# Optimization experiments

Hardware: AMD Instinct MI355X
Metric: run time of the kernel (lower is better)

## Reference

```python
import jax, jax.numpy as jnp
import numpy as np

D_MODEL = 1024
N_HEADS = 16
HEAD_DIM = D_MODEL // N_HEADS  # 64
WINDOW = 64
HALF = WINDOW // 2  # query i attends keys in [i-HALF, i+HALF]
CHUNK = WINDOW      # chunk size for banded attention; must be >= HALF and divide S
B, S = 4, 4096


def setup_inputs() -> dict:
    key = jax.random.key(0)
    ks = jax.random.split(key, 6)
    s = 0.02
    D = D_MODEL
    return {
        "x":  jax.random.normal(ks[0], (B, S, D), jnp.float32),
        "Wq": jax.random.normal(ks[1], (D, D), jnp.float32) * s,
        "bq": jnp.zeros((D,), jnp.float32),
        "Wk": jax.random.normal(ks[2], (D, D), jnp.float32) * s,
        "bk": jnp.zeros((D,), jnp.float32),
        "Wv": jax.random.normal(ks[3], (D, D), jnp.float32) * s,
        "bv": jnp.zeros((D,), jnp.float32),
        "Wo": jax.random.normal(ks[4], (D, D), jnp.float32) * s,
        "bo": jnp.zeros((D,), jnp.float32),
    }


def reference(x, Wq, bq, Wk, bk, Wv, bv, Wo, bo):
    # Sliding-window attention (seq_len > 128 path of SparseAttention).
    b, s, d = x.shape
    h, hd = N_HEADS, HEAD_DIM
    scale = 1.0 / np.sqrt(hd).astype(np.float32)

    q = (x @ Wq.T + bq).reshape(b, s, h, hd)
    k = (x @ Wk.T + bk).reshape(b, s, h, hd)
    v = (x @ Wv.T + bv).reshape(b, s, h, hd)

    c = CHUNK
    nb = s // c
    qc = q.reshape(b, nb, c, h, hd)

    # Pad one chunk of zeros on each side; each query chunk attends keys in
    # chunks [n-1, n, n+1] (covers the +/-HALF band since HALF <= c).
    pad = jnp.zeros((b, c, h, hd), q.dtype)
    kp = jnp.concatenate([pad, k, pad], axis=1).reshape(b, nb + 2, c, h, hd)
    vp = jnp.concatenate([pad, v, pad], axis=1).reshape(b, nb + 2, c, h, hd)
    k3 = jnp.concatenate([kp[:, :-2], kp[:, 1:-1], kp[:, 2:]], axis=2)  # [b,nb,3c,h,hd]
    v3 = jnp.concatenate([vp[:, :-2], vp[:, 1:-1], vp[:, 2:]], axis=2)

    # scores: [b,h,nb,c,3c]
    scores = jnp.einsum('bnqhd,bnkhd->bhnqk', qc, k3) * scale

    # Banded validity mask. Global query pos = n*c + i ; global key pos = n*c + j - c.
    i = jnp.arange(c)[:, None]          # [c,1]
    j = jnp.arange(3 * c)[None, :]      # [1,3c]
    rel = j - c - i                     # key_pos - query_pos, [c,3c]
    band = (rel >= -HALF) & (rel <= HALF)
    n = jnp.arange(nb)[:, None, None]   # [nb,1,1]
    keypos = n * c + (j - c)[None, :, :]  # [nb,1,3c]
    valid = band[None, :, :] & (keypos >= 0) & (keypos < s)  # [nb,c,3c]

    attn = jax.nn.softmax(jnp.where(valid[None, None], scores, -jnp.inf), axis=-1)
    ctx = jnp.einsum('bhnqk,bnkhd->bnqhd', attn, v3).reshape(b, s, d)
    return ctx @ Wo.T + bo
```

## Files before the change

kernel.cpp:

```cpp
#include <hip/hip_runtime.h>
#include <hip/hip_bf16.h>
#include <cstdint>
#include <cstddef>

#define D_MODEL 1024
#define NHEADS  16
#define HDIM    64
#define HALFW   32
#define BATCH   4
#define SEQ     4096
#define MROWS   (BATCH*SEQ)

typedef __attribute__((ext_vector_type(8))) short        bf16x8;
typedef __attribute__((ext_vector_type(4))) float        f32x4;
typedef __attribute__((ext_vector_type(4))) unsigned int u32x4;

typedef const __attribute__((address_space(1))) void gvoid_t;
typedef __attribute__((address_space(3))) void       lvoid_t;

__device__ __forceinline__ unsigned short f2bf(float f) {
    unsigned int u = __float_as_uint(f);
    u += 0x7fffu + ((u >> 16) & 1u);
    return (unsigned short)(u >> 16);
}

__device__ __forceinline__ int vswz(int row, int bytecol) {
    return (row * 256 + bytecol) ^ (((row ^ (row >> 3)) & 7) << 4);
}

__global__ __launch_bounds__(256)
void cvt_f32_bf16(const float* __restrict__ src, unsigned short* __restrict__ dst, int n8) {
    int i = blockIdx.x * 256 + threadIdx.x;
    if (i >= n8) return;
    float4 a = *(const float4*)(src + (size_t)i * 8);
    float4 b = *(const float4*)(src + (size_t)i * 8 + 4);
    u32x4 o;
    o[0] = (unsigned)f2bf(a.x) | ((unsigned)f2bf(a.y) << 16);
    o[1] = (unsigned)f2bf(a.z) | ((unsigned)f2bf(a.w) << 16);
    o[2] = (unsigned)f2bf(b.x) | ((unsigned)f2bf(b.y) << 16);
    o[3] = (unsigned)f2bf(b.z) | ((unsigned)f2bf(b.w) << 16);
    *(u32x4*)(dst + (size_t)i * 8) = o;
}

__global__ __launch_bounds__(256)
void cvt4_f32_bf16(const float* __restrict__ s0, const float* __restrict__ s1,
                   const float* __restrict__ s2, const float* __restrict__ s3,
                   unsigned short* __restrict__ d0, unsigned short* __restrict__ d1,
                   unsigned short* __restrict__ d2, unsigned short* __restrict__ d3, int n8) {
    int i = blockIdx.x * 256 + threadIdx.x;
    if (i >= n8) return;
    const float* src = blockIdx.y == 0 ? s0 : blockIdx.y == 1 ? s1 : blockIdx.y == 2 ? s2 : s3;
    unsigned short* dst = blockIdx.y == 0 ? d0 : blockIdx.y == 1 ? d1 : blockIdx.y == 2 ? d2 : d3;
    float4 a = *(const float4*)(src + (size_t)i * 8);
    float4 b = *(const float4*)(src + (size_t)i * 8 + 4);
    u32x4 o;
    o[0] = (unsigned)f2bf(a.x) | ((unsigned)f2bf(a.y) << 16);
    o[1] = (unsigned)f2bf(a.z) | ((unsigned)f2bf(a.w) << 16);
    o[2] = (unsigned)f2bf(b.x) | ((unsigned)f2bf(b.y) << 16);
    o[3] = (unsigned)f2bf(b.z) | ((unsigned)f2bf(b.w) << 16);
    *(u32x4*)(dst + (size_t)i * 8) = o;
}

template <int NOUT, int F32OUT>
__global__ __launch_bounds__(512)
void gemm256(const unsigned short* __restrict__ A,
             const unsigned short* __restrict__ W0,
             const unsigned short* __restrict__ W1,
             const unsigned short* __restrict__ W2,
             const float* __restrict__ b0, const float* __restrict__ b1,
             const float* __restrict__ b2,
             unsigned short* __restrict__ o0, unsigned short* __restrict__ o1,
             unsigned short* __restrict__ o2, float* __restrict__ of32)
{
    constexpr int K  = 1024;
    constexpr int NT = K / 64;
    constexpr int NWG = 64 * 4 * NOUT;
    __shared__ unsigned short lds[65536];

    const int tid  = threadIdx.x;
    const int wave = tid >> 6, lane = tid & 63;
    const int wr = wave >> 2, wc = wave & 3;

    const int bid = blockIdx.x;
    const int g   = (bid & 7) * (NWG / 8) + (bid >> 3);
    const int rb  = g / (4 * NOUT);
    const int cb  = g % (4 * NOUT);
    const int which = cb >> 2;
    const int bm = rb * 256, bn = (cb & 3) * 256;

    const unsigned short* W = (NOUT == 1 || which == 0) ? W0 : (which == 1 ? W1 : W2);
    const float* bias       = (NOUT == 1 || which == 0) ? b0 : (which == 1 ? b1 : b2);
    unsigned short* obf     = (NOUT == 1 || which == 0) ? o0 : (which == 1 ? o1 : o2);

    f32x4 acc[8][4];
    #pragma unroll
    for (int m = 0; m < 8; ++m)
        #pragma unroll
        for (int n = 0; n < 4; ++n)
            #pragma unroll
            for (int j = 0; j < 4; ++j) acc[m][n][j] = 0.0f;

    char* ldsb = (char*)lds;

    const int idx0 = tid, idx1 = tid + 512;
    const int r0 = idx0 >> 2, r1 = idx1 >> 2;
    const int c0 = ((idx0 & 3) - (r0 >> 1)) & 3;
    const int c1 = ((idx1 & 3) - (r1 >> 1)) & 3;
    const size_t sA0 = (size_t)(bm + r0) * K + c0 * 8;
    const size_t sA1 = (size_t)(bm + r1) * K + c1 * 8;
    const size_t sB0 = (size_t)(bn + r0) * K + c0 * 8;
    const size_t sB1 = (size_t)(bn + r1) * K + c1 * 8;
    const int ldsW = wave * 1024;

    auto STAGE = [&](int t, int kh, int isA) {
        const int slot = ((t << 1) + kh) & 3;
        const int base = (isA ? 0 : 65536) + slot * 16384 + ldsW;
        const int ke = t * 64 + kh * 32;
        const unsigned short* M = isA ? A : W;
        const size_t s0 = isA ? sA0 : sB0;
        const size_t s1 = isA ? sA1 : sB1;
        __builtin_amdgcn_global_load_lds((gvoid_t*)(M + s0 + ke),
            (lvoid_t*)(ldsb + base), 16, 0, 0);
        __builtin_amdgcn_global_load_lds((gvoid_t*)(M + s1 + ke),
            (lvoid_t*)(ldsb + base + 8192), 16, 0, 0);
    };

    const int lr = lane & 15;
    const int pp = (((lane >> 4) + (lr >> 1)) & 3) << 4;
    const int abase = (wr * 128 + lr) * 64 + pp;
    const int bbase = 65536 + (wc * 64 + lr) * 64 + pp;

    STAGE(0, 0, 1); STAGE(0, 0, 0); STAGE(0, 1, 1); STAGE(0, 1, 0);
    asm volatile("s_waitcnt vmcnt(4)" ::: "memory");
    __builtin_amdgcn_s_barrier();

    #pragma unroll 1
    for (int t = 0; t < NT; ++t) {
        const int more = (t + 1 < NT);
        {
            const int so = (((t << 1) + 0) & 3) * 16384;
            if (more) STAGE(t + 1, 0, 1);
            bf16x8 a[8], b2_[2];
            #pragma unroll
            for (int m = 0; m < 8; ++m) a[m] = *(const bf16x8*)(ldsb + so + abase + m * 1024);
            #pragma unroll
            for (int n = 0; n < 2; ++n) b2_[n] = *(const bf16x8*)(ldsb + so + bbase + n * 1024);
            __builtin_amdgcn_s_barrier();
            __builtin_amdgcn_s_setprio(1);
            #pragma unroll
            for (int m = 0; m < 8; ++m)
                #pragma unroll
                for (int n = 0; n < 2; ++n)
                    acc[m][n] = __builtin_amdgcn_mfma_f32_16x16x32_bf16(a[m], b2_[n], acc[m][n], 0, 0, 0);
            __builtin_amdgcn_s_setprio(0);
            __builtin_amdgcn_s_barrier();
            if (more) STAGE(t + 1, 0, 0);
            #pragma unroll
            for (int n = 0; n < 2; ++n) b2_[n] = *(const bf16x8*)(ldsb + so + bbase + (n + 2) * 1024);
            __builtin_amdgcn_s_barrier();
            __builtin_amdgcn_s_setprio(1);
            #pragma unroll
            for (int m = 0; m < 8; ++m)
                #pragma unroll
                for (int n = 0; n < 2; ++n)
                    acc[m][n + 2] = __builtin_amdgcn_mfma_f32_16x16x32_bf16(a[m], b2_[n], acc[m][n + 2], 0, 0, 0);
            __builtin_amdgcn_s_setprio(0);
            if (more) { asm volatile("s_waitcnt vmcnt(4)" ::: "memory"); }
            else      { asm volatile("s_waitcnt vmcnt(0)" ::: "memory"); }
            __builtin_amdgcn_s_barrier();
        }
        {
            const int so = (((t << 1) + 1) & 3) * 16384;
            if (more) STAGE(t + 1, 1, 1);
            bf16x8 a[8], b2_[2];
            #pragma unroll
            for (int m = 0; m < 8; ++m) a[m] = *(const bf16x8*)(ldsb + so + abase + m * 1024);
            #pragma unroll
            for (int n = 0; n < 2; ++n) b2_[n] = *(const bf16x8*)(ldsb + so + bbase + n * 1024);
            __builtin_amdgcn_s_barrier();
            __builtin_amdgcn_s_setprio(1);
            #pragma unroll
            for (int m = 0; m < 8; ++m)
                #pragma unroll
                for (int n = 0; n < 2; ++n)
                    acc[m][n] = __builtin_amdgcn_mfma_f32_16x16x32_bf16(a[m], b2_[n], acc[m][n], 0, 0, 0);
            __builtin_amdgcn_s_setprio(0);
            __builtin_amdgcn_s_barrier();
            if (more) STAGE(t + 1, 1, 0);
            #pragma unroll
            for (int n = 0; n < 2; ++n) b2_[n] = *(const bf16x8*)(ldsb + so + bbase + (n + 2) * 1024);
            __builtin_amdgcn_s_barrier();
            __builtin_amdgcn_s_setprio(1);
            #pragma unroll
            for (int m = 0; m < 8; ++m)
                #pragma unroll
                for (int n = 0; n < 2; ++n)
                    acc[m][n + 2] = __builtin_amdgcn_mfma_f32_16x16x32_bf16(a[m], b2_[n], acc[m][n + 2], 0, 0, 0);
            __builtin_amdgcn_s_setprio(0);
            if (t + 2 < NT) { asm volatile("s_waitcnt vmcnt(4)" ::: "memory"); }
            else            { asm volatile("s_waitcnt vmcnt(0)" ::: "memory"); }
            __builtin_amdgcn_s_barrier();
        }
    }

    float bvv[4];
    #pragma unroll
    for (int n = 0; n < 4; ++n) bvv[n] = bias[bn + wc * 64 + n * 16 + lr];
    #pragma unroll
    for (int m = 0; m < 8; ++m) {
        #pragma unroll
        for (int j = 0; j < 4; ++j) {
            const int row = bm + wr * 128 + m * 16 + (lane >> 4) * 4 + j;
            #pragma unroll
            for (int n = 0; n < 4; ++n) {
                const int col = bn + wc * 64 + n * 16 + lr;
                const float v = acc[m][n][j] + bvv[n];
                if (F32OUT) of32[(size_t)row * 1024 + col] = v;
                else        obf[(size_t)row * 1024 + col]  = f2bf(v);
            }
        }
    }
}

__global__ __launch_bounds__(256)
void attn_band(const unsigned short* __restrict__ Q,
               const unsigned short* __restrict__ Kk,
               const unsigned short* __restrict__ V,
               unsigned short* __restrict__ Ctx)
{
    __shared__ unsigned short Qs[64 * 72];
    __shared__ unsigned short Ks[128 * 72];
    __shared__ unsigned short Vt[64 * 128];
    __shared__ unsigned short Ps[64 * 128];

    const int qt = blockIdx.x, h = blockIdx.y, b = blockIdx.z;
    const int qbase  = qt * 64;
    const int kstart = qbase - HALFW;
    const int tid = threadIdx.x, wave = tid >> 6, lane = tid & 63;

    const size_t base = (size_t)b * SEQ * D_MODEL + (size_t)h * HDIM;
    const unsigned short* Qb = Q  + base;
    const unsigned short* Kb = Kk + base;
    const unsigned short* Vb = V  + base;
    unsigned short*       Cb = Ctx + base;

    for (int c = tid; c < 512; c += 256) {
        const int row = c >> 3, col = (c & 7) * 8;
        *(u32x4*)(Qs + row * 72 + col) =
            *(const u32x4*)(Qb + (size_t)(qbase + row) * D_MODEL + col);
    }
    for (int c = tid; c < 1024; c += 256) {
        const int krow = c >> 3, col = (c & 7) * 8;
        const int kpos = kstart + krow;
        u32x4 kv;
        if (kpos >= 0 && kpos < SEQ) {
            kv = *(const u32x4*)(Kb + (size_t)kpos * D_MODEL + col);
        } else {
            for (int j = 0; j < 4; ++j) kv[j] = 0u;
        }
        *(u32x4*)(Ks + krow * 72 + col) = kv;
    }
    for (int c = tid; c < 512; c += 256) {
        const int p = c >> 3, dch = c & 7;
        const int k0 = kstart + 2 * p, k1 = k0 + 1;
        u32x4 v0, v1;
        if (k0 >= 0 && k0 < SEQ) {
            v0 = *(const u32x4*)(Vb + (size_t)k0 * D_MODEL + dch * 8);
        } else {
            for (int j = 0; j < 4; ++j) v0[j] = 0u;
        }
        if (k1 >= 0 && k1 < SEQ) {
            v1 = *(const u32x4*)(Vb + (size_t)k1 * D_MODEL + dch * 8);
        } else {
            for (int j = 0; j < 4; ++j) v1[j] = 0u;
        }
        #pragma unroll
        for (int j = 0; j < 8; ++j) {
            const int d = dch * 8 + j;
            const unsigned lo = (v0[j >> 1] >> ((j & 1) * 16)) & 0xffffu;
            const unsigned hi = (v1[j >> 1] >> ((j & 1) * 16)) & 0xffffu;
            *(unsigned*)((char*)Vt + vswz(d, 4 * p)) = lo | (hi << 16);
        }
    }
    __syncthreads();

    f32x4 sc[8];
    #pragma unroll
    for (int c = 0; c < 8; ++c)
        #pragma unroll
        for (int j = 0; j < 4; ++j) sc[c][j] = 0.0f;

    bf16x8 aq[2];
    #pragma unroll
    for (int kc = 0; kc < 2; ++kc)
        aq[kc] = *(const bf16x8*)(Qs + (wave * 16 + (lane & 15)) * 72 + kc * 32 + (lane >> 4) * 8);
    #pragma unroll
    for (int c = 0; c < 8; ++c) {
        #pragma unroll
        for (int kc = 0; kc < 2; ++kc) {
            bf16x8 bk_ = *(const bf16x8*)(Ks + (c * 16 + (lane & 15)) * 72 + kc * 32 + (lane >> 4) * 8);
            sc[c] = __builtin_amdgcn_mfma_f32_16x16x32_bf16(aq[kc], bk_, sc[c], 0, 0, 0);
        }
    }

    const int grp = lane >> 4, colk = lane & 15;
    float rowmax[4] = {-1e30f, -1e30f, -1e30f, -1e30f};
    #pragma unroll
    for (int c = 0; c < 8; ++c) {
        const int kpos = kstart + c * 16 + colk;
        #pragma unroll
        for (int j = 0; j < 4; ++j) {
            const int qpos = qbase + wave * 16 + grp * 4 + j;
            const int rel = kpos - qpos;
            const bool valid = (kpos >= 0) && (kpos < SEQ) && (rel >= -HALFW) && (rel <= HALFW);
            const float v = valid ? sc[c][j] * 0.125f : -1e30f;
            sc[c][j] = v;
            rowmax[j] = fmaxf(rowmax[j], v);
        }
    }
    #pragma unroll
    for (int j = 0; j < 4; ++j)
        #pragma unroll
        for (int m = 1; m < 16; m <<= 1)
            rowmax[j] = fmaxf(rowmax[j], __shfl_xor(rowmax[j], m, 64));

    float rowsum[4] = {0.f, 0.f, 0.f, 0.f};
    #pragma unroll
    for (int c = 0; c < 8; ++c)
        #pragma unroll
        for (int j = 0; j < 4; ++j) {
            const float p = __expf(sc[c][j] - rowmax[j]);
            sc[c][j] = p;
            rowsum[j] += p;
        }
    #pragma unroll
    for (int j = 0; j < 4; ++j)
        #pragma unroll
        for (int m = 1; m < 16; m <<= 1)
            rowsum[j] += __shfl_xor(rowsum[j], m, 64);

    #pragma unroll
    for (int c = 0; c < 8; ++c)
        #pragma unroll
        for (int j = 0; j < 4; ++j)
            *(unsigned short*)((char*)Ps + vswz(wave * 16 + grp * 4 + j, (c * 16 + colk) * 2))
                = f2bf(sc[c][j]);
    __syncthreads();

    f32x4 o[4];
    #pragma unroll
    for (int n = 0; n < 4; ++n)
        #pragma unroll
        for (int j = 0; j < 4; ++j) o[n][j] = 0.0f;
    #pragma unroll
    for (int kc = 0; kc < 4; ++kc) {
        bf16x8 pa = *(const bf16x8*)((const char*)Ps +
                        vswz(wave * 16 + (lane & 15), kc * 64 + (lane >> 4) * 16));
        #pragma unroll
        for (int n = 0; n < 4; ++n) {
            bf16x8 bv_ = *(const bf16x8*)((const char*)Vt +
                            vswz(n * 16 + (lane & 15), kc * 64 + (lane >> 4) * 16));
            o[n] = __builtin_amdgcn_mfma_f32_16x16x32_bf16(pa, bv_, o[n], 0, 0, 0);
        }
    }

    float rinv[4];
    #pragma unroll
    for (int j = 0; j < 4; ++j) rinv[j] = 1.0f / rowsum[j];
    #pragma unroll
    for (int n = 0; n < 4; ++n)
        #pragma unroll
        for (int j = 0; j < 4; ++j) {
            const int q = qbase + wave * 16 + grp * 4 + j;
            Cb[(size_t)q * D_MODEL + n * 16 + colk] = f2bf(o[n][j] * rinv[j]);
        }
}

extern "C" void kernel_launch(void* const* d_in, const int* in_sizes, int n_in,
                              void* d_out, int out_size, void* d_ws, size_t ws_size,
                              hipStream_t stream)
{
    (void)in_sizes; (void)n_in; (void)out_size; (void)ws_size;
    const float* x  = (const float*)d_in[0];
    const float* Wq = (const float*)d_in[1];
    const float* bq = (const float*)d_in[2];
    const float* Wk = (const float*)d_in[3];
    const float* bk = (const float*)d_in[4];
    const float* Wv = (const float*)d_in[5];
    const float* bv = (const float*)d_in[6];
    const float* Wo = (const float*)d_in[7];
    const float* bo = (const float*)d_in[8];
    float* out = (float*)d_out;

    char* ws = (char*)d_ws;
    unsigned short* xb  = (unsigned short*)ws;
    unsigned short* wqb = (unsigned short*)(ws + 33554432);
    unsigned short* wkb = wqb + 1048576;
    unsigned short* wvb = wkb + 1048576;
    unsigned short* wob = wvb + 1048576;
    unsigned short* qb  = wob + 1048576;
    unsigned short* kb  = qb + (size_t)MROWS * D_MODEL;
    unsigned short* vb  = kb + (size_t)MROWS * D_MODEL;
    unsigned short* ctxb = xb;

    cvt_f32_bf16<<<dim3(MROWS * D_MODEL / 8 / 256), 256, 0, stream>>>(x, xb, MROWS * D_MODEL / 8);
    cvt4_f32_bf16<<<dim3(D_MODEL * D_MODEL / 8 / 256, 4), 256, 0, stream>>>(
        Wq, Wk, Wv, Wo, wqb, wkb, wvb, wob, D_MODEL * D_MODEL / 8);

    gemm256<3, 0><<<dim3(768), 512, 0, stream>>>(
        xb, wqb, wkb, wvb, bq, bk, bv, qb, kb, vb, nullptr);

    attn_band<<<dim3(SEQ / 64, NHEADS, BATCH), 256, 0, stream>>>(qb, kb, vb, ctxb);

    gemm256<1, 1><<<dim3(256), 512, 0, stream>>>(
        ctxb, wob, wob, wob, bo, bo, bo, nullptr, nullptr, nullptr, out);
}
```

Before: 232.2 us.

## Deepen GEMM LDS pipeline to three half-tiles in flight with split-M MFMA phases

Restructures the bf16 GEMM main loop to iterate over 32-wide K half-tiles with a prefetch distance of three slots in the four-slot LDS ring, instead of one tile ahead. Each iteration loads all four B fragments once and splits the MFMA work by M halves (rows 0-3, then 4-7), with sched_barriers and explicit lgkmcnt/vmcnt waits to pin the order. The aim is to hide more global-load latency and cut LDS re-reads of B fragments. In exchange, the vmcnt tail logic is more complex and ordering mistakes could cause stalls or races.

```diff
diff --git a/kernel.cpp b/kernel.cpp
--- a/kernel.cpp
+++ b/kernel.cpp
@@ -73,7 +73,7 @@
              unsigned short* __restrict__ o2, float* __restrict__ of32)
 {
     constexpr int K  = 1024;
-    constexpr int NT = K / 64;
+    constexpr int HT = K / 32;
     constexpr int NWG = 64 * 4 * NOUT;
     __shared__ unsigned short lds[65536];
 
@@ -112,10 +112,9 @@
     const size_t sB1 = (size_t)(bn + r1) * K + c1 * 8;
     const int ldsW = wave * 1024;
 
-    auto STAGE = [&](int t, int kh, int isA) {
-        const int slot = ((t << 1) + kh) & 3;
-        const int base = (isA ? 0 : 65536) + slot * 16384 + ldsW;
-        const int ke = t * 64 + kh * 32;
+    auto STAGE = [&](int h, int isA) {
+        const int base = (isA ? 0 : 65536) + (h & 3) * 16384 + ldsW;
+        const int ke = h * 32;
         const unsigned short* M = isA ? A : W;
         const size_t s0 = isA ? sA0 : sB0;
         const size_t s1 = isA ? sA1 : sB1;
@@ -130,77 +129,53 @@
     const int abase = (wr * 128 + lr) * 64 + pp;
     const int bbase = 65536 + (wc * 64 + lr) * 64 + pp;
 
-    STAGE(0, 0, 1); STAGE(0, 0, 0); STAGE(0, 1, 1); STAGE(0, 1, 0);
-    asm volatile("s_waitcnt vmcnt(4)" ::: "memory");
+    STAGE(0, 1); STAGE(0, 0); STAGE(1, 1); STAGE(1, 0); STAGE(2, 1); STAGE(2, 0);
+    asm volatile("s_waitcnt vmcnt(8)" ::: "memory");
     __builtin_amdgcn_s_barrier();
 
     #pragma unroll 1
-    for (int t = 0; t < NT; ++t) {
-        const int more = (t + 1 < NT);
-        {
-            const int so = (((t << 1) + 0) & 3) * 16384;
-            if (more) STAGE(t + 1, 0, 1);
-            bf16x8 a[8], b2_[2];
+    for (int hp = 0; hp < HT; ++hp) {
+        const int so = (hp & 3) * 16384;
+        bf16x8 aL[4], bb[4], aH[4];
+        #pragma unroll
+        for (int m = 0; m < 4; ++m) aL[m] = *(const bf16x8*)(ldsb + so + abase + m * 1024);
+        #pragma unroll
+        for (int n = 0; n < 4; ++n) bb[n] = *(const bf16x8*)(ldsb + so + bbase + n * 1024);
+        __builtin_amdgcn_sched_barrier(0);
+        if (hp + 3 < HT) STAGE(hp + 3, 1);
+        __builtin_amdgcn_sched_barrier(0);
+        __builtin_amdgcn_s_barrier();
+        asm volatile("s_waitcnt lgkmcnt(0)" ::: "memory");
+        __builtin_amdgcn_sched_barrier(0);
+        __builtin_amdgcn_s_setprio(1);
+        #pragma unroll
+        for (int m = 0; m < 4; ++m)
             #pragma unroll
-            for (int m = 0; m < 8; ++m) a[m] = *(const bf16x8*)(ldsb + so + abase + m * 1024);
+            for (int n = 0; n < 4; ++n)
+                acc[m][n] = __builtin_amdgcn_mfma_f32_16x16x32_bf16(aL[m], bb[n], acc[m][n], 0, 0, 0);
+        __builtin_amdgcn_s_setprio(0);
+        __builtin_amdgcn_sched_barrier(0);
+        __builtin_amdgcn_s_barrier();
+        #pragma unroll
+        for (int m = 0; m < 4; ++m) aH[m] = *(const bf16x8*)(ldsb + so + abase + (m + 4) * 1024);
+        __builtin_amdgcn_sched_barrier(0);
+        if (hp + 3 < HT) STAGE(hp + 3, 0);
+        if (hp <= HT - 4)      { asm volatile("s_waitcnt vmcnt(8)" ::: "memory"); }
+        else if (hp == HT - 3) { asm volatile("s_waitcnt vmcnt(4)" ::: "memory"); }
+        else if (hp == HT - 2) { asm volatile("s_waitcnt vmcnt(0)" ::: "memory"); }
+        __builtin_amdgcn_sched_barrier(0);
+        __builtin_amdgcn_s_barrier();
+        asm volatile("s_waitcnt lgkmcnt(0)" ::: "memory");
+        __builtin_amdgcn_sched_barrier(0);
+        __builtin_amdgcn_s_setprio(1);
+        #pragma unroll
+        for (int m = 0; m < 4; ++m)
             #pragma unroll
-            for (int n = 0; n < 2; ++n) b2_[n] = *(const bf16x8*)(ldsb + so + bbase + n * 1024);
-            __builtin_amdgcn_s_barrier();
-            __builtin_amdgcn_s_setprio(1);
-            #pragma unroll
-            for (int m = 0; m < 8; ++m)
-                #pragma unroll
-                for (int n = 0; n < 2; ++n)
-                    acc[m][n] = __builtin_amdgcn_mfma_f32_16x16x32_bf16(a[m], b2_[n], acc[m][n], 0, 0, 0);
-            __builtin_amdgcn_s_setprio(0);
-            __builtin_amdgcn_s_barrier();
-            if (more) STAGE(t + 1, 0, 0);
-            #pragma unroll
-            for (int n = 0; n < 2; ++n) b2_[n] = *(const bf16x8*)(ldsb + so + bbase + (n + 2) * 1024);
-            __builtin_amdgcn_s_barrier();
-            __builtin_amdgcn_s_setprio(1);
-            #pragma unroll
-            for (int m = 0; m < 8; ++m)
-                #pragma unroll
-                for (int n = 0; n < 2; ++n)
-                    acc[m][n + 2] = __builtin_amdgcn_mfma_f32_16x16x32_bf16(a[m], b2_[n], acc[m][n + 2], 0, 0, 0);
-            __builtin_amdgcn_s_setprio(0);
-            if (more) { asm volatile("s_waitcnt vmcnt(4)" ::: "memory"); }
-            else      { asm volatile("s_waitcnt vmcnt(0)" ::: "memory"); }
-            __builtin_amdgcn_s_barrier();
-        }
-        {
-            const int so = (((t << 1) + 1) & 3) * 16384;
-            if (more) STAGE(t + 1, 1, 1);
-            bf16x8 a[8], b2_[2];
-            #pragma unroll
-            for (int m = 0; m < 8; ++m) a[m] = *(const bf16x8*)(ldsb + so + abase + m * 1024);
-            #pragma unroll
-            for (int n = 0; n < 2; ++n) b2_[n] = *(const bf16x8*)(ldsb + so + bbase + n * 1024);
-            __builtin_amdgcn_s_barrier();
-            __builtin_amdgcn_s_setprio(1);
-            #pragma unroll
-            for (int m = 0; m < 8; ++m)
-                #pragma unroll
-                for (int n = 0; n < 2; ++n)
-                    acc[m][n] = __builtin_amdgcn_mfma_f32_16x16x32_bf16(a[m], b2_[n], acc[m][n], 0, 0, 0);
-            __builtin_amdgcn_s_setprio(0);
-            __builtin_amdgcn_s_barrier();
-            if (more) STAGE(t + 1, 1, 0);
-            #pragma unroll
-            for (int n = 0; n < 2; ++n) b2_[n] = *(const bf16x8*)(ldsb + so + bbase + (n + 2) * 1024);
-            __builtin_amdgcn_s_barrier();
-            __builtin_amdgcn_s_setprio(1);
-            #pragma unroll
-            for (int m = 0; m < 8; ++m)
-                #pragma unroll
-                for (int n = 0; n < 2; ++n)
-                    acc[m][n + 2] = __builtin_amdgcn_mfma_f32_16x16x32_bf16(a[m], b2_[n], acc[m][n + 2], 0, 0, 0);
-            __builtin_amdgcn_s_setprio(0);
-            if (t + 2 < NT) { asm volatile("s_waitcnt vmcnt(4)" ::: "memory"); }
-            else            { asm volatile("s_waitcnt vmcnt(0)" ::: "memory"); }
-            __builtin_amdgcn_s_barrier();
-        }
+            for (int n = 0; n < 4; ++n)
+                acc[m + 4][n] = __builtin_amdgcn_mfma_f32_16x16x32_bf16(aH[m], bb[n], acc[m + 4][n], 0, 0, 0);
+        __builtin_amdgcn_s_setprio(0);
+        __builtin_amdgcn_sched_barrier(0);
+        __builtin_amdgcn_s_barrier();
     }
 
     float bvv[4];
```

After: 238.1 us. 1.03x slower.
